# Performance work log

Measured on AMD Instinct MI355X. Metric: run time of the kernel, lower is better.

## Reference

```python
import jax, jax.numpy as jnp
import numpy as np

N, NFEAT, NHID = 10000, 512, 128


def setup_inputs() -> dict:
    key = jax.random.key(0)
    k_x, k_adj, k_w1, k_b1, k_w2, k_b2 = jax.random.split(key, 6)
    x = jax.random.normal(k_x, (N, NFEAT), dtype=jnp.float32)
    # dense normalized adjacency (affinity matrix, as built by aff_to_adj in the repo)
    adj = jax.random.uniform(k_adj, (N, N), dtype=jnp.float32)
    # Kipf GraphConvolution init: uniform(-1/sqrt(out), 1/sqrt(out))
    s1 = 1.0 / np.sqrt(NHID)
    s2 = 1.0 / np.sqrt(NFEAT)
    W1 = jax.random.uniform(k_w1, (NFEAT, NHID), minval=-s1, maxval=s1, dtype=jnp.float32)
    b1 = jax.random.uniform(k_b1, (NHID,), minval=-s1, maxval=s1, dtype=jnp.float32)
    W2 = jax.random.uniform(k_w2, (NHID, NFEAT), minval=-s2, maxval=s2, dtype=jnp.float32)
    b2 = jax.random.uniform(k_b2, (NFEAT,), minval=-s2, maxval=s2, dtype=jnp.float32)
    return {"x": x, "adj": adj, "W1": W1, "b1": b1, "W2": W2, "b2": b2}


def reference(x, adj, W1, b1, W2, b2):
    # gc1: adj @ (x @ W1) + b1, then ReLU
    h = jax.nn.relu(adj @ (x @ W1) + b1)          # [N, NHID]
    # dropout is identity in eval mode (training=False)
    # gc2: adj @ (h @ W2) + b2
    out = adj @ (h @ W2) + b2                      # [N, NFEAT]
    return out
```

## Files before the change

### kernel.cpp

```cpp
#include <hip/hip_runtime.h>
#include <stdint.h>

typedef __bf16 bf16x8 __attribute__((ext_vector_type(8)));
typedef float  f32x4  __attribute__((ext_vector_type(4)));

__device__ __forceinline__ void gl_lds16(const void* g, void* l) {
  __builtin_amdgcn_global_load_lds(
      (const __attribute__((address_space(1))) void*)g,
      (__attribute__((address_space(3))) void*)l, 16, 0, 0);
}

__global__ void transpose_cvt(const float* __restrict__ in, __bf16* __restrict__ out,
                              int R, int Ccols) {
  int idx = blockIdx.x * 256 + threadIdx.x;
  if (idx < R * Ccols) {
    int r = idx / Ccols, c = idx % Ccols;
    out[(size_t)c * R + r] = (__bf16)in[(size_t)r * Ccols + c];
  }
}

__global__ void reduce_sk(const float* __restrict__ P, int S, int MN,
                          const float* __restrict__ bias, __bf16* __restrict__ out,
                          int do_relu, int transT, int ldT) {
  int idx = blockIdx.x * 256 + threadIdx.x;
  if (idx >= MN) return;
  float v = 0.0f;
  for (int s = 0; s < S; ++s) v += P[(size_t)s * MN + idx];
  int col = idx & 127, row = idx >> 7;
  if (bias) v += bias[col];
  if (do_relu && v < 0.0f) v = 0.0f;
  if (transT) out[(size_t)col * ldT + row] = (__bf16)v;
  else        out[idx] = (__bf16)v;
}

template<bool AF32, int MODE>
__global__ __launch_bounds__(256) void gemm_sk(
    const void* __restrict__ A, int lda,
    const __bf16* __restrict__ BT, int ldbt,
    void* __restrict__ C, int ldc,
    const float* __restrict__ bias,
    int M, int N, int K, int kchunk, int do_relu, int transC)
{
  constexpr int ABYTES = AF32 ? 16384 : 8192;
  constexpr int BUFB = ABYTES + 8192;
  __shared__ char smem[2 * BUFB];

  const int tid  = threadIdx.x;
  const int lane = tid & 63;
  const int w    = tid >> 6;
  const int wr = w >> 1, wc = w & 1;
  const int quad = lane >> 4, l15 = lane & 15;

  const int mblk = blockIdx.x * 128;
  const int nblk = blockIdx.y * 128;
  const int kbeg = blockIdx.z * kchunk;
  int kend = kbeg + kchunk; if (kend > K) kend = K;

  f32x4 acc[4][4] = {};

  auto stage = [&](int buf, int kt) {
    char* sA = smem + buf * BUFB;
    char* sB = sA + ABYTES;
    const int klen = (kend - kt) < 32 ? (kend - kt) : 32;
    if (AF32) {
      const float* Af = (const float*)A;
      #pragma unroll
      for (int t = 0; t < 4; ++t) {
        int slot = (w * 4 + t) * 64 + lane;
        int row = slot >> 3, p = slot & 7;
        int u = p ^ (row & 7);
        int rg = mblk + row; if (rg >= M) rg = M - 1;
        int ku = (u * 4 + 4 <= klen) ? (kt + u * 4) : kt;
        gl_lds16(Af + (size_t)rg * lda + ku, sA + slot * 16);
      }
    } else {
      const __bf16* Ab = (const __bf16*)A;
      #pragma unroll
      for (int t = 0; t < 2; ++t) {
        int slot = (w * 2 + t) * 64 + lane;
        int row = slot >> 2, p = slot & 3;
        int u = p ^ (row & 3);
        int rg = mblk + row; if (rg >= M) rg = M - 1;
        int ku = (u * 8 + 8 <= klen) ? (kt + u * 8) : kt;
        gl_lds16(Ab + (size_t)rg * lda + ku, sA + slot * 16);
      }
    }
    #pragma unroll
    for (int t = 0; t < 2; ++t) {
      int slot = (w * 2 + t) * 64 + lane;
      int row = slot >> 2, p = slot & 3;
      int u = p ^ (row & 3);
      int rg = nblk + row; if (rg >= N) rg = N - 1;
      int ku = (u * 8 + 8 <= klen) ? (kt + u * 8) : kt;
      gl_lds16(BT + (size_t)rg * ldbt + ku, sB + slot * 16);
    }
  };

  int cur = 0;
  stage(0, kbeg);
  asm volatile("s_waitcnt vmcnt(0)" ::: "memory");
  __builtin_amdgcn_s_barrier();
  asm volatile("" ::: "memory");

  for (int kt = kbeg; kt < kend; kt += 32) {
    if (kt + 32 < kend) stage(cur ^ 1, kt + 32);

    const int klen = (kend - kt) < 32 ? (kend - kt) : 32;
    char* sA = smem + cur * BUFB;
    char* sB = sA + ABYTES;

    bf16x8 af[4], bfr[4];
    #pragma unroll
    for (int i = 0; i < 4; ++i) {
      int mloc = wr * 64 + i * 16 + l15;
      if (AF32) {
        int u0 = quad * 2, u1 = u0 + 1;
        f32x4 lo = *(const f32x4*)(sA + mloc * 128 + ((u0 ^ (mloc & 7)) * 16));
        f32x4 hi = *(const f32x4*)(sA + mloc * 128 + ((u1 ^ (mloc & 7)) * 16));
        bf16x8 r;
        r[0] = (__bf16)lo[0]; r[1] = (__bf16)lo[1]; r[2] = (__bf16)lo[2]; r[3] = (__bf16)lo[3];
        r[4] = (__bf16)hi[0]; r[5] = (__bf16)hi[1]; r[6] = (__bf16)hi[2]; r[7] = (__bf16)hi[3];
        af[i] = r;
      } else {
        af[i] = *(const bf16x8*)(sA + mloc * 64 + ((quad ^ (mloc & 3)) * 16));
      }
    }
    #pragma unroll
    for (int j = 0; j < 4; ++j) {
      int nloc = wc * 64 + j * 16 + l15;
      bfr[j] = *(const bf16x8*)(sB + nloc * 64 + ((quad ^ (nloc & 3)) * 16));
    }
    if (klen < 32) {
      bf16x8 z = {};
      if (quad * 8 + 8 > klen) {
        #pragma unroll
        for (int i = 0; i < 4; ++i) af[i] = z;
      }
    }
    #pragma unroll
    for (int i = 0; i < 4; ++i)
      #pragma unroll
      for (int j = 0; j < 4; ++j)
        acc[i][j] = __builtin_amdgcn_mfma_f32_16x16x32_bf16(af[i], bfr[j], acc[i][j], 0, 0, 0);

    asm volatile("s_waitcnt vmcnt(0)" ::: "memory");
    __builtin_amdgcn_s_barrier();
    asm volatile("" ::: "memory");
    cur ^= 1;
  }

  if (MODE == 0) {
    float* P = (float*)C + (size_t)blockIdx.z * ((size_t)M * N);
    #pragma unroll
    for (int j = 0; j < 4; ++j) {
      int col = nblk + wc * 64 + j * 16 + l15;
      #pragma unroll
      for (int i = 0; i < 4; ++i) {
        int rowb = mblk + wr * 64 + i * 16 + quad * 4;
        #pragma unroll
        for (int r = 0; r < 4; ++r) {
          int row = rowb + r;
          if (row < M) P[(size_t)row * N + col] = acc[i][j][r];
        }
      }
    }
  } else {
    #pragma unroll
    for (int j = 0; j < 4; ++j) {
      int col = nblk + wc * 64 + j * 16 + l15;
      float bv = bias ? bias[col] : 0.0f;
      #pragma unroll
      for (int i = 0; i < 4; ++i) {
        int rowb = mblk + wr * 64 + i * 16 + quad * 4;
        #pragma unroll
        for (int r = 0; r < 4; ++r) {
          int row = rowb + r;
          if (row < M) {
            float v = acc[i][j][r] + bv;
            if (do_relu && v < 0.0f) v = 0.0f;
            size_t idx = transC ? ((size_t)col * ldc + row) : ((size_t)row * ldc + col);
            if (MODE == 1) ((__bf16*)C)[idx] = (__bf16)v;
            else           ((float*)C)[idx] = v;
          }
        }
      }
    }
  }
}

extern "C" void kernel_launch(void* const* d_in, const int* in_sizes, int n_in,
                              void* d_out, int out_size, void* d_ws, size_t ws_size,
                              hipStream_t stream) {
  const float* x   = (const float*)d_in[0];
  const float* adj = (const float*)d_in[1];
  const float* W1  = (const float*)d_in[2];
  const float* b1  = (const float*)d_in[3];
  const float* W2  = (const float*)d_in[4];
  const float* b2  = (const float*)d_in[5];
  float* out = (float*)d_out;

  const int Nn = 10000, NF = 512, NH = 128;
  const size_t MN = (size_t)Nn * NH;

  char* ws = (char*)d_ws;
  __bf16* W1T = (__bf16*)(ws + 0);
  __bf16* W2T = (__bf16*)(ws + 131072);
  __bf16* xwT = (__bf16*)(ws + 262144);
  __bf16* hT  = (__bf16*)(ws + 2822144);
  __bf16* ah  = (__bf16*)(ws + 5382144);
  float*  P   = (float*)(ws + 7942144);

  size_t slab = MN * sizeof(float);
  long avail = (long)((ws_size - 7942144) / slab);
  int S = avail < 1 ? 1 : (avail > 16 ? 16 : (int)avail);
  int kchunk = ((Nn + S - 1) / S + 31) & ~31;
  int Sz = (Nn + kchunk - 1) / kchunk;

  dim3 blk(256);
  const int MB = (Nn + 127) / 128;

  hipLaunchKernelGGL(transpose_cvt, dim3((NF * NH + 255) / 256), blk, 0, stream, W1, W1T, NF, NH);
  hipLaunchKernelGGL(transpose_cvt, dim3((NF * NH + 255) / 256), blk, 0, stream, W2, W2T, NH, NF);

  hipLaunchKernelGGL((gemm_sk<true, 1>), dim3(MB, 1, 1), blk, 0, stream,
                     (const void*)x, NF, W1T, NF, (void*)xwT, Nn, (const float*)nullptr,
                     Nn, NH, NF, NF, 0, 1);
  hipLaunchKernelGGL((gemm_sk<true, 0>), dim3(MB, 1, Sz), blk, 0, stream,
                     (const void*)adj, Nn, xwT, Nn, (void*)P, NH, (const float*)nullptr,
                     Nn, NH, Nn, kchunk, 0, 0);
  hipLaunchKernelGGL(reduce_sk, dim3(((int)MN + 255) / 256), blk, 0, stream,
                     P, Sz, (int)MN, b1, hT, 1, 1, Nn);
  hipLaunchKernelGGL((gemm_sk<true, 0>), dim3(MB, 1, Sz), blk, 0, stream,
                     (const void*)adj, Nn, hT, Nn, (void*)P, NH, (const float*)nullptr,
                     Nn, NH, Nn, kchunk, 0, 0);
  hipLaunchKernelGGL(reduce_sk, dim3(((int)MN + 255) / 256), blk, 0, stream,
                     P, Sz, (int)MN, (const float*)nullptr, ah, 0, 0, 0);
  hipLaunchKernelGGL((gemm_sk<false, 2>), dim3(MB, 4, 1), blk, 0, stream,
                     (const void*)ah, NH, W2T, NH, (void*)out, NF, b2,
                     Nn, NF, NH, NH, 0, 0);
}
```

Before: 794.0 us.

## Replace split-K adjacency GEMMs with 16-row tiles and fused epilogue

Drops split-K partial sums and the separate reduction kernels. Each adjacency GEMM now uses 16x128 output tiles over the full K, giving 625 blocks, and writes bias/ReLU/bf16 output directly from the epilogue. This removes the fp32 partial-slab writes and reads plus two extra launches. In exchange each block reloads the full B operand (xwT/hT) for every 16 rows, which raises L2 traffic for B, and the MFMA work per LDS load drops.

Result: slower. 941.2 us (+18.5%).

```diff
diff --git a/kernel.cpp b/kernel.cpp
--- a/kernel.cpp
+++ b/kernel.cpp
@@ -2,6 +2,7 @@
 #include <stdint.h>
 
 typedef __bf16 bf16x8 __attribute__((ext_vector_type(8)));
+typedef __bf16 bf16x4 __attribute__((ext_vector_type(4)));
 typedef float  f32x4  __attribute__((ext_vector_type(4)));
 
 __device__ __forceinline__ void gl_lds16(const void* g, void* l) {
@@ -19,77 +20,58 @@
   }
 }
 
-__global__ void reduce_sk(const float* __restrict__ P, int S, int MN,
-                          const float* __restrict__ bias, __bf16* __restrict__ out,
-                          int do_relu, int transT, int ldT) {
-  int idx = blockIdx.x * 256 + threadIdx.x;
-  if (idx >= MN) return;
-  float v = 0.0f;
-  for (int s = 0; s < S; ++s) v += P[(size_t)s * MN + idx];
-  int col = idx & 127, row = idx >> 7;
-  if (bias) v += bias[col];
-  if (do_relu && v < 0.0f) v = 0.0f;
-  if (transT) out[(size_t)col * ldT + row] = (__bf16)v;
-  else        out[idx] = (__bf16)v;
-}
-
 template<bool AF32, int MODE>
-__global__ __launch_bounds__(256) void gemm_sk(
+__global__ __launch_bounds__(256) void gemm16(
     const void* __restrict__ A, int lda,
     const __bf16* __restrict__ BT, int ldbt,
     void* __restrict__ C, int ldc,
     const float* __restrict__ bias,
-    int M, int N, int K, int kchunk, int do_relu, int transC)
+    int M, int N, int K, int do_relu, int transC)
 {
-  constexpr int ABYTES = AF32 ? 16384 : 8192;
-  constexpr int BUFB = ABYTES + 8192;
+  constexpr int ABYTES = AF32 ? 4096 : 2048;
+  constexpr int BBYTES = 16384;
+  constexpr int BUFB = ABYTES + BBYTES;
   __shared__ char smem[2 * BUFB];
 
   const int tid  = threadIdx.x;
   const int lane = tid & 63;
   const int w    = tid >> 6;
-  const int wr = w >> 1, wc = w & 1;
   const int quad = lane >> 4, l15 = lane & 15;
 
-  const int mblk = blockIdx.x * 128;
+  const int mblk = blockIdx.x * 16;
   const int nblk = blockIdx.y * 128;
-  const int kbeg = blockIdx.z * kchunk;
-  int kend = kbeg + kchunk; if (kend > K) kend = K;
+  const int kend = K;
 
-  f32x4 acc[4][4] = {};
+  f32x4 acc[2] = {};
 
   auto stage = [&](int buf, int kt) {
     char* sA = smem + buf * BUFB;
     char* sB = sA + ABYTES;
-    const int klen = (kend - kt) < 32 ? (kend - kt) : 32;
+    const int klen = (kend - kt) < 64 ? (kend - kt) : 64;
     if (AF32) {
       const float* Af = (const float*)A;
-      #pragma unroll
-      for (int t = 0; t < 4; ++t) {
-        int slot = (w * 4 + t) * 64 + lane;
+      int slot = tid;
+      int row = slot >> 4, p = slot & 15;
+      int u = p ^ row;
+      int rg = mblk + row; if (rg >= M) rg = M - 1;
+      int ku = (u * 4 + 4 <= klen) ? (kt + u * 4) : kt;
+      gl_lds16(Af + (size_t)rg * lda + ku, sA + slot * 16);
+    } else {
+      if (w < 2) {
+        const __bf16* Ab = (const __bf16*)A;
+        int slot = w * 64 + lane;
         int row = slot >> 3, p = slot & 7;
         int u = p ^ (row & 7);
-        int rg = mblk + row; if (rg >= M) rg = M - 1;
-        int ku = (u * 4 + 4 <= klen) ? (kt + u * 4) : kt;
-        gl_lds16(Af + (size_t)rg * lda + ku, sA + slot * 16);
-      }
-    } else {
-      const __bf16* Ab = (const __bf16*)A;
-      #pragma unroll
-      for (int t = 0; t < 2; ++t) {
-        int slot = (w * 2 + t) * 64 + lane;
-        int row = slot >> 2, p = slot & 3;
-        int u = p ^ (row & 3);
         int rg = mblk + row; if (rg >= M) rg = M - 1;
         int ku = (u * 8 + 8 <= klen) ? (kt + u * 8) : kt;
         gl_lds16(Ab + (size_t)rg * lda + ku, sA + slot * 16);
       }
     }
     #pragma unroll
-    for (int t = 0; t < 2; ++t) {
-      int slot = (w * 2 + t) * 64 + lane;
-      int row = slot >> 2, p = slot & 3;
-      int u = p ^ (row & 3);
+    for (int t = 0; t < 4; ++t) {
+      int slot = (w * 4 + t) * 64 + lane;
+      int row = slot >> 3, p = slot & 7;
+      int u = p ^ (row & 7);
       int rg = nblk + row; if (rg >= N) rg = N - 1;
       int ku = (u * 8 + 8 <= klen) ? (kt + u * 8) : kt;
       gl_lds16(BT + (size_t)rg * ldbt + ku, sB + slot * 16);
@@ -97,51 +79,42 @@
   };
 
   int cur = 0;
-  stage(0, kbeg);
+  stage(0, 0);
   asm volatile("s_waitcnt vmcnt(0)" ::: "memory");
   __builtin_amdgcn_s_barrier();
   asm volatile("" ::: "memory");
 
-  for (int kt = kbeg; kt < kend; kt += 32) {
-    if (kt + 32 < kend) stage(cur ^ 1, kt + 32);
+  for (int kt = 0; kt < kend; kt += 64) {
+    if (kt + 64 < kend) stage(cur ^ 1, kt + 64);
 
-    const int klen = (kend - kt) < 32 ? (kend - kt) : 32;
+    const int klen = (kend - kt) < 64 ? (kend - kt) : 64;
     char* sA = smem + cur * BUFB;
     char* sB = sA + ABYTES;
 
-    bf16x8 af[4], bfr[4];
     #pragma unroll
-    for (int i = 0; i < 4; ++i) {
-      int mloc = wr * 64 + i * 16 + l15;
+    for (int ks = 0; ks < 2; ++ks) {
+      bf16x8 af;
       if (AF32) {
-        int u0 = quad * 2, u1 = u0 + 1;
-        f32x4 lo = *(const f32x4*)(sA + mloc * 128 + ((u0 ^ (mloc & 7)) * 16));
-        f32x4 hi = *(const f32x4*)(sA + mloc * 128 + ((u1 ^ (mloc & 7)) * 16));
-        bf16x8 r;
-        r[0] = (__bf16)lo[0]; r[1] = (__bf16)lo[1]; r[2] = (__bf16)lo[2]; r[3] = (__bf16)lo[3];
-        r[4] = (__bf16)hi[0]; r[5] = (__bf16)hi[1]; r[6] = (__bf16)hi[2]; r[7] = (__bf16)hi[3];
-        af[i] = r;
+        int uw0 = ks * 8 + quad * 2;
+        f32x4 lo = *(const f32x4*)(sA + l15 * 256 + ((uw0 ^ l15) * 16));
+        f32x4 hi = *(const f32x4*)(sA + l15 * 256 + (((uw0 + 1) ^ l15) * 16));
+        af[0] = (__bf16)lo[0]; af[1] = (__bf16)lo[1]; af[2] = (__bf16)lo[2]; af[3] = (__bf16)lo[3];
+        af[4] = (__bf16)hi[0]; af[5] = (__bf16)hi[1]; af[6] = (__bf16)hi[2]; af[7] = (__bf16)hi[3];
       } else {
-        af[i] = *(const bf16x8*)(sA + mloc * 64 + ((quad ^ (mloc & 3)) * 16));
+        int uw = ks * 4 + quad;
+        af = *(const bf16x8*)(sA + l15 * 128 + ((uw ^ (l15 & 7)) * 16));
+      }
+      if (ks * 32 + quad * 8 + 8 > klen) {
+        bf16x8 z = {};
+        af = z;
+      }
+      #pragma unroll
+      for (int jj = 0; jj < 2; ++jj) {
+        int nloc = w * 32 + jj * 16 + l15;
+        bf16x8 bfr = *(const bf16x8*)(sB + nloc * 128 + (((ks * 4 + quad) ^ (nloc & 7)) * 16));
+        acc[jj] = __builtin_amdgcn_mfma_f32_16x16x32_bf16(af, bfr, acc[jj], 0, 0, 0);
       }
     }
-    #pragma unroll
-    for (int j = 0; j < 4; ++j) {
-      int nloc = wc * 64 + j * 16 + l15;
-      bfr[j] = *(const bf16x8*)(sB + nloc * 64 + ((quad ^ (nloc & 3)) * 16));
-    }
-    if (klen < 32) {
-      bf16x8 z = {};
-      if (quad * 8 + 8 > klen) {
-        #pragma unroll
-        for (int i = 0; i < 4; ++i) af[i] = z;
-      }
-    }
-    #pragma unroll
-    for (int i = 0; i < 4; ++i)
-      #pragma unroll
-      for (int j = 0; j < 4; ++j)
-        acc[i][j] = __builtin_amdgcn_mfma_f32_16x16x32_bf16(af[i], bfr[j], acc[i][j], 0, 0, 0);
 
     asm volatile("s_waitcnt vmcnt(0)" ::: "memory");
     __builtin_amdgcn_s_barrier();
@@ -149,39 +122,34 @@
     cur ^= 1;
   }
 
-  if (MODE == 0) {
-    float* P = (float*)C + (size_t)blockIdx.z * ((size_t)M * N);
-    #pragma unroll
-    for (int j = 0; j < 4; ++j) {
-      int col = nblk + wc * 64 + j * 16 + l15;
+  const int rowb = mblk + quad * 4;
+  #pragma unroll
+  for (int jj = 0; jj < 2; ++jj) {
+    int col = nblk + w * 32 + jj * 16 + l15;
+    if (col >= N) continue;
+    float bv = bias ? bias[col] : 0.0f;
+    if (MODE == 1 && transC) {
+      bf16x4 v;
       #pragma unroll
-      for (int i = 0; i < 4; ++i) {
-        int rowb = mblk + wr * 64 + i * 16 + quad * 4;
-        #pragma unroll
-        for (int r = 0; r < 4; ++r) {
-          int row = rowb + r;
-          if (row < M) P[(size_t)row * N + col] = acc[i][j][r];
-        }
+      for (int r = 0; r < 4; ++r) {
+        float f = acc[jj][r] + bv;
+        if (do_relu && f < 0.0f) f = 0.0f;
+        v[r] = (__bf16)f;
       }
-    }
-  } else {
-    #pragma unroll
-    for (int j = 0; j < 4; ++j) {
-      int col = nblk + wc * 64 + j * 16 + l15;
-      float bv = bias ? bias[col] : 0.0f;
+      if (rowb + 3 < M)
+        *(bf16x4*)((__bf16*)C + (size_t)col * ldc + rowb) = v;
+      else
+        for (int r = 0; r < 4; ++r)
+          if (rowb + r < M) ((__bf16*)C)[(size_t)col * ldc + rowb + r] = v[r];
+    } else {
       #pragma unroll
-      for (int i = 0; i < 4; ++i) {
-        int rowb = mblk + wr * 64 + i * 16 + quad * 4;
-        #pragma unroll
-        for (int r = 0; r < 4; ++r) {
-          int row = rowb + r;
-          if (row < M) {
-            float v = acc[i][j][r] + bv;
-            if (do_relu && v < 0.0f) v = 0.0f;
-            size_t idx = transC ? ((size_t)col * ldc + row) : ((size_t)row * ldc + col);
-            if (MODE == 1) ((__bf16*)C)[idx] = (__bf16)v;
-            else           ((float*)C)[idx] = v;
-          }
+      for (int r = 0; r < 4; ++r) {
+        int row = rowb + r;
+        if (row < M) {
+          float f = acc[jj][r] + bv;
+          if (do_relu && f < 0.0f) f = 0.0f;
+          if (MODE == 1) ((__bf16*)C)[(size_t)row * ldc + col] = (__bf16)f;
+          else           ((float*)C)[(size_t)row * ldc + col] = f;
         }
       }
     }
@@ -200,7 +168,6 @@
   float* out = (float*)d_out;
 
   const int Nn = 10000, NF = 512, NH = 128;
-  const size_t MN = (size_t)Nn * NH;
 
   char* ws = (char*)d_ws;
   __bf16* W1T = (__bf16*)(ws + 0);
@@ -208,34 +175,24 @@
   __bf16* xwT = (__bf16*)(ws + 262144);
   __bf16* hT  = (__bf16*)(ws + 2822144);
   __bf16* ah  = (__bf16*)(ws + 5382144);
-  float*  P   = (float*)(ws + 7942144);
-
-  size_t slab = MN * sizeof(float);
-  long avail = (long)((ws_size - 7942144) / slab);
-  int S = avail < 1 ? 1 : (avail > 16 ? 16 : (int)avail);
-  int kchunk = ((Nn + S - 1) / S + 31) & ~31;
-  int Sz = (Nn + kchunk - 1) / kchunk;
+  (void)ws_size;
 
   dim3 blk(256);
-  const int MB = (Nn + 127) / 128;
+  const int MB = Nn / 16;
 
   hipLaunchKernelGGL(transpose_cvt, dim3((NF * NH + 255) / 256), blk, 0, stream, W1, W1T, NF, NH);
   hipLaunchKernelGGL(transpose_cvt, dim3((NF * NH + 255) / 256), blk, 0, stream, W2, W2T, NH, NF);
 
-  hipLaunchKernelGGL((gemm_sk<true, 1>), dim3(MB, 1, 1), blk, 0, stream,
+  hipLaunchKernelGGL((gemm16<true, 1>), dim3(MB, 1), blk, 0, stream,
                      (const void*)x, NF, W1T, NF, (void*)xwT, Nn, (const float*)nullptr,
-                     Nn, NH, NF, NF, 0, 1);
-  hipLaunchKernelGGL((gemm_sk<true, 0>), dim3(MB, 1, Sz), blk, 0, stream,
-                     (const void*)adj, Nn, xwT, Nn, (void*)P, NH, (const float*)nullptr,
-                     Nn, NH, Nn, kchunk, 0, 0);
-  hipLaunchKernelGGL(reduce_sk, dim3(((int)MN + 255) / 256), blk, 0, stream,
-                     P, Sz, (int)MN, b1, hT, 1, 1, Nn);
-  hipLaunchKernelGGL((gemm_sk<true, 0>), dim3(MB, 1, Sz), blk, 0, stream,
-                     (const void*)adj, Nn, hT, Nn, (void*)P, NH, (const float*)nullptr,
-                     Nn, NH, Nn, kchunk, 0, 0);
-  hipLaunchKernelGGL(reduce_sk, dim3(((int)MN + 255) / 256), blk, 0, stream,
-                     P, Sz, (int)MN, (const float*)nullptr, ah, 0, 0, 0);
-  hipLaunchKernelGGL((gemm_sk<false, 2>), dim3(MB, 4, 1), blk, 0, stream,
+                     Nn, NH, NF, 0, 1);
+  hipLaunchKernelGGL((gemm16<true, 1>), dim3(MB, 1), blk, 0, stream,
+                     (const void*)adj, Nn, xwT, Nn, (void*)hT, Nn, b1,
+                     Nn, NH, Nn, 1, 1);
+  hipLaunchKernelGGL((gemm16<true, 1>), dim3(MB, 1), blk, 0, stream,
+                     (const void*)adj, Nn, hT, Nn, (void*)ah, NH, (const float*)nullptr,
+                     Nn, NH, Nn, 0, 0);
+  hipLaunchKernelGGL((gemm16<false, 2>), dim3(MB, 4), blk, 0, stream,
                      (const void*)ah, NH, W2T, NH, (void*)out, NF, b2,
-                     Nn, NF, NH, NH, 0, 0);
+                     Nn, NF, NH, 0, 0);
 }
```
